# Kernel optimization log

Measured on AMD Instinct MI355X. Metric: run time of the kernel, lower is better.

The kernel has to match this reference:

```python
import jax, jax.numpy as jnp
import numpy as np

# --- SLAYER hyperparameters (from netParams) ---
THETA = 10.0        # spike threshold
TAU_SR = 10.0       # SRM alpha-kernel time constant (ms)
TAU_RHO = 1.0       # surrogate-gradient width
SCALE_RHO = 1.0     # surrogate-gradient scale
TS = 1.0            # simulation step (ms)
T_SAMPLE = 300      # number of time steps
K_LEN = 64          # truncated SRM kernel length

N_BATCH, N_IN, N_HID, N_OUT = 128, 784, 410, 10


def srm_kernel():
    # SRM-alpha kernel eps(t) = (t/tau) * exp(1 - t/tau), sampled at Ts, eps(0)=0
    t = jnp.arange(K_LEN, dtype=jnp.float32) * TS
    return (t / TAU_SR) * jnp.exp(1.0 - t / TAU_SR)


def psp(x):
    # Causal FIR filtering along time: out[t] = sum_k eps[k] * x[t-k]
    # x: [N, C, T]
    n, c, t = x.shape
    kern = srm_kernel()
    lhs = x.reshape(n * c, 1, t)
    rhs = kern[::-1].reshape(1, 1, K_LEN)  # flip: conv_general_dilated is cross-correlation
    out = jax.lax.conv_general_dilated(
        lhs, rhs, window_strides=(1,), padding=[(K_LEN - 1, 0)],
        dimension_numbers=("NCH", "OIH", "NCH"))
    return out.reshape(n, c, t)


@jax.custom_vjp
def spike_fn(u):
    # Heaviside threshold with surrogate gradient rho(u) = (scale/tau) * exp(-|u-theta|/tau)
    return (u >= THETA).astype(u.dtype)

def _spike_fwd(u):
    return spike_fn(u), u

def _spike_bwd(u, g):
    return (g * (SCALE_RHO / TAU_RHO) * jnp.exp(-jnp.abs(u - THETA) / TAU_RHO),)

spike_fn.defvjp(_spike_fwd, _spike_bwd)


def setup_inputs() -> dict:
    key = jax.random.key(0)
    k1, k2, k3, k4 = jax.random.split(key, 4)
    img = jax.random.uniform(k1, (N_BATCH, N_IN), dtype=jnp.float32)
    rand_u = jax.random.uniform(k2, (N_BATCH, N_IN, T_SAMPLE), dtype=jnp.float32)
    W1 = jax.random.normal(k3, (N_HID, N_IN), dtype=jnp.float32)
    W2 = jax.random.normal(k4, (N_OUT, N_HID), dtype=jnp.float32)
    return {"img": img, "rand_u": rand_u, "W1": W1, "W2": W2}


def reference(img, rand_u, W1, W2):
    # Poisson spike encoding: spike whenever uniform noise < pixel intensity
    s0 = (rand_u < img[:, :, None]).astype(jnp.float32)        # [N, 784, T]
    # fc1 (dense over spatial features, shared over time) -> psp -> spike
    a1 = jnp.einsum("nit,oi->not", s0, W1)                     # [N, 410, T]
    s1 = spike_fn(psp(a1))
    # fc2 -> psp -> spike
    a2 = jnp.einsum("nht,oh->not", s1, W2)                     # [N, 10, T]
    s2 = spike_fn(psp(a2))
    return s2
```

## Files before the change

### kernel.cpp

```cpp
#include <hip/hip_runtime.h>
#include <cstdint>
#include <cstddef>

#define N_B 128
#define N_I 784
#define N_H 410
#define N_O 10
#define TT  300
#define KL  64
#define NK  832
#define NKS 13
#define NTILES 26
#define NDIG 4
#define NKS2 7
#define S1_TILE 4800
#define S1_NSTRIDE 134400
#define SEGL 19
#define NWG1 (NTILES * N_B)
#define WPX  (NWG1 / 8)

typedef int v4i __attribute__((ext_vector_type(4)));

__global__ void k_pack(const float* __restrict__ rand_u, const float* __restrict__ img,
                       uint8_t* __restrict__ s0b) {
  int t = blockIdx.x * 64 + threadIdx.x;
  int w2 = blockIdx.y;
  int n = blockIdx.z;
  if (t >= TT) return;
  const float* rb = rand_u + (size_t)n * N_I * TT + t;
  const float* ib = img + (size_t)n * N_I;
  uint8_t* dst = s0b + ((size_t)n * TT + t) * NK + w2 * 64;
  int kb = w2 * 64;
  #pragma unroll
  for (int g = 0; g < 4; ++g) {
    uint32_t wd[4];
    #pragma unroll
    for (int q = 0; q < 4; ++q) {
      uint32_t v = 0;
      #pragma unroll
      for (int b = 0; b < 4; ++b) {
        int i = kb + g * 16 + q * 4 + b;
        float r = (i < N_I) ? rb[(size_t)i * TT] : 2.0f;
        float p = (i < N_I) ? ib[i] : 0.0f;
        v |= (r < p ? 1u : 0u) << (8 * b);
      }
      wd[q] = v;
    }
    v4i o; o[0] = (int)wd[0]; o[1] = (int)wd[1]; o[2] = (int)wd[2]; o[3] = (int)wd[3];
    *(v4i*)(dst + g * 16) = o;
  }
}

__global__ void k_bprepall(const float* __restrict__ W1, const float* __restrict__ W2,
                           v4i* __restrict__ Bf, v4i* __restrict__ Bf2) {
  int bid  = blockIdx.x;
  int lane = threadIdx.x;
  if (bid < NDIG * NTILES * NKS) {
    int ks   = bid % NKS;
    int rest = bid / NKS;
    int nt   = rest % NTILES;
    int d    = rest / NTILES;
    int o     = nt * 16 + (lane & 15);
    int kbase = ks * 64 + (lane >> 4) * 16;
    uint32_t wds[4] = {0, 0, 0, 0};
    for (int j = 0; j < 16; ++j) {
      int k = kbase + j;
      int dig = 0;
      if (o < N_H && k < N_I) {
        double w = (double)W1[(size_t)o * N_I + k];
        int r = (int)llround(w * 268435456.0);
        for (int dd = 0; dd <= d; ++dd) {
          dig = (int)(int8_t)(uint8_t)(r & 255);
          r = (r - dig) >> 8;
        }
      }
      wds[j >> 2] |= ((uint32_t)(uint8_t)(int8_t)dig) << (8 * (j & 3));
    }
    v4i v; v[0] = (int)wds[0]; v[1] = (int)wds[1]; v[2] = (int)wds[2]; v[3] = (int)wds[3];
    Bf[(size_t)bid * 64 + lane] = v;
  } else {
    int b2 = bid - NDIG * NTILES * NKS;
    int ks = b2 % NKS2, d = b2 / NKS2;
    int o     = lane & 15;
    int kbase = ks * 64 + (lane >> 4) * 16;
    uint32_t wds[4] = {0, 0, 0, 0};
    for (int j = 0; j < 16; ++j) {
      int k = kbase + j;
      int dig = 0;
      if (o < N_O && k < N_H) {
        double w = (double)W2[(size_t)o * N_H + k];
        int r = (int)llround(w * 268435456.0);
        for (int dd = 0; dd <= d; ++dd) {
          dig = (int)(int8_t)(uint8_t)(r & 255);
          r = (r - dig) >> 8;
        }
      }
      wds[j >> 2] |= ((uint32_t)(uint8_t)(int8_t)dig) << (8 * (j & 3));
    }
    v4i v; v[0] = (int)wds[0]; v[1] = (int)wds[1]; v[2] = (int)wds[2]; v[3] = (int)wds[3];
    Bf2[(size_t)b2 * 64 + lane] = v;
  }
}

__global__ __launch_bounds__(256) void k_fused2(const uint8_t* __restrict__ s0b,
                                                const v4i* __restrict__ Bf,
                                                uint8_t* __restrict__ s1) {
  __shared__ double tile[TT][17];
  int tid = threadIdx.x;
  int wave = tid >> 6, lane = tid & 63;
  int bid = blockIdx.x;
  int sw = (bid & 7) * WPX + (bid >> 3);
  int n = sw / NTILES, nt = sw % NTILES;
  int lrow = lane & 15, quad = lane >> 4;
  const v4i* bb = Bf + (size_t)nt * NKS * 64 + lane;
  const size_t dstr = (size_t)NTILES * NKS * 64;
  const uint8_t* an = s0b + (size_t)n * TT * NK + quad * 16;

  v4i acc[5][NDIG];
  #pragma unroll
  for (int mti = 0; mti < 5; ++mti)
    #pragma unroll
    for (int d = 0; d < NDIG; ++d) { acc[mti][d][0]=0; acc[mti][d][1]=0; acc[mti][d][2]=0; acc[mti][d][3]=0; }
  const uint8_t* ap[5];
  #pragma unroll
  for (int mti = 0; mti < 5; ++mti) {
    int rr = wave * 80 + mti * 16 + lrow;
    if (rr > TT - 1) rr = TT - 1;
    ap[mti] = an + (size_t)rr * NK;
  }
  v4i bcur[NDIG], acur[5];
  #pragma unroll
  for (int d = 0; d < NDIG; ++d) bcur[d] = bb[d * dstr];
  #pragma unroll
  for (int mti = 0; mti < 5; ++mti) acur[mti] = *(const v4i*)ap[mti];
  for (int ks = 0; ks < NKS; ++ks) {
    int ks2 = (ks + 1 < NKS) ? ks + 1 : ks;
    v4i bnxt[NDIG], anxt[5];
    #pragma unroll
    for (int d = 0; d < NDIG; ++d) bnxt[d] = bb[d * dstr + ks2 * 64];
    #pragma unroll
    for (int mti = 0; mti < 5; ++mti) anxt[mti] = *(const v4i*)(ap[mti] + ks2 * 64);
    #pragma unroll
    for (int mti = 0; mti < 5; ++mti)
      #pragma unroll
      for (int d = 0; d < NDIG; ++d)
        acc[mti][d] = __builtin_amdgcn_mfma_i32_16x16x64_i8(acur[mti], bcur[d], acc[mti][d], 0, 0, 0);
    #pragma unroll
    for (int d = 0; d < NDIG; ++d) bcur[d] = bnxt[d];
    #pragma unroll
    for (int mti = 0; mti < 5; ++mti) acur[mti] = anxt[mti];
  }
  #pragma unroll
  for (int mti = 0; mti < 5; ++mti)
    #pragma unroll
    for (int r = 0; r < 4; ++r) {
      int m = wave * 80 + mti * 16 + quad * 4 + r;
      if (m < TT) {
        double v = (double)acc[mti][0][r]
                 + 256.0      * (double)acc[mti][1][r]
                 + 65536.0    * (double)acc[mti][2][r]
                 + 16777216.0 * (double)acc[mti][3][r];
        tile[m][lrow] = v;
      }
    }
  __syncthreads();

  {
    int col = tid & 15;
    int seg = tid >> 4;
    int T0 = seg * SEGL;
    int Wc = T0 - 63; if (Wc < 0) Wc = 0;
    const double q   = exp(-0.1);
    const double q64 = exp(-6.4);
    const double cS  = (exp(1.0) / 10.0) * (1.0 / 268435456.0);
    double s1a = 0.0, s2a = 0.0, s1b = 0.0, s2b = 0.0;
    uint8_t* sb = s1 + (size_t)n * S1_NSTRIDE + (size_t)nt * S1_TILE + col;
    for (int j = 0; j < 63; ++j) {
      int t = T0 - 63 + j;
      int tc = (t < 0) ? 0 : t;
      double xa = (t >= 0) ? tile[tc][col] : 0.0;
      s2a = q * (s2a + s1a);
      s1a = q * s1a + xa;
    }
    for (int j = 0; j < SEGL; ++j) {
      int t = T0 + j;
      int tc = (t > TT - 1) ? TT - 1 : t;
      int tb = t - 64;
      int tbc = (tb < 0) ? 0 : tb;
      double xa = tile[tc][col];
      double xb = (tb >= Wc) ? tile[tbc][col] : 0.0;
      s2b = q * (s2b + s1b);
      s1b = q * s1b + xb;
      s2a = q * (s2a + s1a);
      s1a = q * s1a + xa;
      double y = cS * (s2a - q64 * (s2b + 64.0 * s1b));
      if (t < TT) sb[(size_t)t * 16] = (y >= 10.0) ? 1 : 0;
    }
  }
}

__global__ __launch_bounds__(256) void k_l2f(const uint8_t* __restrict__ s1,
                                             const v4i* __restrict__ Bf2,
                                             float* __restrict__ out) {
  __shared__ double tile2[TT][17];
  int tid = threadIdx.x;
  int wave = tid >> 6, lane = tid & 63;
  int n = blockIdx.x;
  int lrow = lane & 15, quad = lane >> 4;
  const uint8_t* s1n = s1 + (size_t)n * S1_NSTRIDE;
  for (int mt = wave; mt < 19; mt += 4) {
    int m0 = mt * 16;
    int trow = m0 + lrow; if (trow > TT - 1) trow = TT - 1;
    v4i acc[NDIG];
    #pragma unroll
    for (int d = 0; d < NDIG; ++d) { acc[d][0]=0; acc[d][1]=0; acc[d][2]=0; acc[d][3]=0; }
    for (int ks = 0; ks < NKS2; ++ks) {
      v4i af = *(const v4i*)(s1n + (size_t)(ks * 4 + quad) * S1_TILE + (size_t)trow * 16);
      #pragma unroll
      for (int d = 0; d < NDIG; ++d) {
        v4i bf = Bf2[(size_t)(d * NKS2 + ks) * 64 + lane];
        acc[d] = __builtin_amdgcn_mfma_i32_16x16x64_i8(af, bf, acc[d], 0, 0, 0);
      }
    }
    #pragma unroll
    for (int r = 0; r < 4; ++r) {
      int m = m0 + quad * 4 + r;
      if (m < TT && lrow < N_O) {
        double v = (double)acc[0][r]
                 + 256.0      * (double)acc[1][r]
                 + 65536.0    * (double)acc[2][r]
                 + 16777216.0 * (double)acc[3][r];
        tile2[m][lrow] = v;
      }
    }
  }
  __syncthreads();

  {
    int col = tid & 15;
    int seg = tid >> 4;
    int T0 = seg * SEGL;
    int Wc = T0 - 63; if (Wc < 0) Wc = 0;
    const double q   = exp(-0.1);
    const double q64 = exp(-6.4);
    const double cS  = (exp(1.0) / 10.0) * (1.0 / 268435456.0);
    double s1a = 0.0, s2a = 0.0, s1b = 0.0, s2b = 0.0;
    float* ob = out + (size_t)n * N_O * TT + (size_t)col * TT;
    for (int j = 0; j < 63; ++j) {
      int t = T0 - 63 + j;
      int tc = (t < 0) ? 0 : t;
      double xa = (t >= 0) ? tile2[tc][col] : 0.0;
      s2a = q * (s2a + s1a);
      s1a = q * s1a + xa;
    }
    for (int j = 0; j < SEGL; ++j) {
      int t = T0 + j;
      int tc = (t > TT - 1) ? TT - 1 : t;
      int tb = t - 64;
      int tbc = (tb < 0) ? 0 : tb;
      double xa = tile2[tc][col];
      double xb = (tb >= Wc) ? tile2[tbc][col] : 0.0;
      s2b = q * (s2b + s1b);
      s1b = q * s1b + xb;
      s2a = q * (s2a + s1a);
      s1a = q * s1a + xa;
      double y = cS * (s2a - q64 * (s2b + 64.0 * s1b));
      if (t < TT && col < N_O) ob[t] = (y >= 10.0) ? 1.0f : 0.0f;
    }
  }
}

extern "C" void kernel_launch(void* const* d_in, const int* in_sizes, int n_in,
                              void* d_out, int out_size, void* d_ws, size_t ws_size,
                              hipStream_t stream) {
  const float* img   = (const float*)d_in[0];
  const float* randu = (const float*)d_in[1];
  const float* W1    = (const float*)d_in[2];
  const float* W2    = (const float*)d_in[3];
  float* out = (float*)d_out;

  char* ws = (char*)d_ws;
  size_t off = 0;
  auto alloc = [&](size_t bytes) -> void* {
    void* p = ws + off;
    off = (off + bytes + 511) & ~(size_t)511;
    return p;
  };
  uint8_t*  s0b = (uint8_t*) alloc((size_t)N_B * TT * NK);
  v4i*      Bf  = (v4i*)     alloc((size_t)NDIG * NTILES * NKS * 64 * 16);
  v4i*      Bf2 = (v4i*)     alloc((size_t)NDIG * NKS2 * 64 * 16);
  uint8_t*  s1  = (uint8_t*) alloc((size_t)N_B * S1_NSTRIDE);
  if (off > ws_size) return;

  k_pack    <<<dim3(5, NKS, N_B), 64, 0, stream>>>(randu, img, s0b);
  k_bprepall<<<dim3(NDIG * NTILES * NKS + NDIG * NKS2), 64, 0, stream>>>(W1, W2, Bf, Bf2);
  k_fused2  <<<dim3(NWG1), 256, 0, stream>>>(s0b, Bf, s1);
  k_l2f     <<<dim3(N_B), 256, 0, stream>>>(s1, Bf2, out);
}
```

Measured before the change: 345.9 us.

## Stage layer-1 operands through LDS with async triple-buffered loads; split layer-2 blocks

The layer-1 int8 MFMA GEMM now fetches A and B fragments with global_load_lds (direct global-to-LDS copies) into double-parity LDS buffers, issued three K-steps ahead, and uses manual vmcnt/lgkmcnt waits so loads overlap the MFMA work. The shared tile buffer is reused as LDS staging, which increases LDS use to 72KB per block and may lower occupancy. Separately, the layer-2 kernel launches two blocks per batch item, each scanning half the time range, to double parallelism at the cost of recomputing the layer-2 GEMM in both halves. The hand-written waitcnt counts carry a correctness risk, since the buffer parity reuse depends on them being exact.

```diff
diff --git a/kernel.cpp b/kernel.cpp
--- a/kernel.cpp
+++ b/kernel.cpp
@@ -16,10 +16,18 @@
 #define S1_TILE 4800
 #define S1_NSTRIDE 134400
 #define SEGL 19
+#define SEGL2 10
 #define NWG1 (NTILES * N_B)
 #define WPX  (NWG1 / 8)
+#define DBYTES (NTILES * NKS * 1024)
 
 typedef int v4i __attribute__((ext_vector_type(4)));
+
+__device__ __forceinline__ void glds16(const void* g, void* l) {
+  __builtin_amdgcn_global_load_lds(
+      (const __attribute__((address_space(1))) uint32_t*)g,
+      (__attribute__((address_space(3))) uint32_t*)l, 16, 0, 0);
+}
 
 __global__ void k_pack(const float* __restrict__ rand_u, const float* __restrict__ img,
                        uint8_t* __restrict__ s0b) {
@@ -105,61 +113,97 @@
 __global__ __launch_bounds__(256) void k_fused2(const uint8_t* __restrict__ s0b,
                                                 const v4i* __restrict__ Bf,
                                                 uint8_t* __restrict__ s1) {
-  __shared__ double tile[TT][17];
+  __shared__ __align__(16) uint8_t smem[73728];
+  uint8_t* bufA = smem;
+  uint8_t* bufB = smem + 40960;
+  double (*tile)[17] = (double (*)[17])smem;
+
   int tid = threadIdx.x;
   int wave = tid >> 6, lane = tid & 63;
   int bid = blockIdx.x;
   int sw = (bid & 7) * WPX + (bid >> 3);
   int n = sw / NTILES, nt = sw % NTILES;
   int lrow = lane & 15, quad = lane >> 4;
-  const v4i* bb = Bf + (size_t)nt * NKS * 64 + lane;
-  const size_t dstr = (size_t)NTILES * NKS * 64;
-  const uint8_t* an = s0b + (size_t)n * TT * NK + quad * 16;
+
+  const uint8_t* an0 = s0b + (size_t)n * TT * NK;
+  int arow = wave * 80 + (lane >> 2);
+  int acol = (lane & 3) * 16;
+  const uint8_t* bfb = (const uint8_t*)Bf + (size_t)nt * NKS * 1024 + (size_t)lane * 16;
+
+  auto STAGE = [&](int k, int par) {
+    uint8_t* ad = bufA + par * 20480 + wave * 5120;
+    #pragma unroll
+    for (int c = 0; c < 5; ++c) {
+      int r = arow + c * 16; if (r > TT - 1) r = TT - 1;
+      glds16(an0 + (size_t)r * NK + (size_t)k * 64 + acol, ad + c * 1024);
+    }
+    uint8_t* bd = bufB + par * 16384 + wave * 4096;
+    #pragma unroll
+    for (int d = 0; d < NDIG; ++d)
+      glds16(bfb + (size_t)d * DBYTES + (size_t)k * 1024, bd + d * 1024);
+  };
+  auto LDA = [&](int par, v4i* a) {
+    const uint8_t* base = bufA + par * 20480 + wave * 5120 + quad * 16;
+    #pragma unroll
+    for (int m = 0; m < 5; ++m)
+      a[m] = *(const v4i*)(base + (size_t)(m * 16 + lrow) * 64);
+  };
+  auto LDB = [&](int par, v4i* b) {
+    const uint8_t* base = bufB + par * 16384 + wave * 4096 + lane * 16;
+    #pragma unroll
+    for (int d = 0; d < NDIG; ++d)
+      b[d] = *(const v4i*)(base + (size_t)d * 1024);
+  };
 
   v4i acc[5][NDIG];
   #pragma unroll
-  for (int mti = 0; mti < 5; ++mti)
-    #pragma unroll
-    for (int d = 0; d < NDIG; ++d) { acc[mti][d][0]=0; acc[mti][d][1]=0; acc[mti][d][2]=0; acc[mti][d][3]=0; }
-  const uint8_t* ap[5];
+  for (int m = 0; m < 5; ++m)
+    #pragma unroll
+    for (int d = 0; d < NDIG; ++d) { acc[m][d][0]=0; acc[m][d][1]=0; acc[m][d][2]=0; acc[m][d][3]=0; }
+
+  STAGE(0, 0);
+  STAGE(1, 1);
+  asm volatile("s_waitcnt vmcnt(9)" ::: "memory");
+  v4i acur[5], bcur[NDIG], anxt[5], bnxt[NDIG];
+  LDA(0, acur); LDB(0, bcur);
+  asm volatile("s_waitcnt lgkmcnt(0)" ::: "memory");
+  __builtin_amdgcn_sched_barrier(0);
+  STAGE(2, 0);
+
   #pragma unroll
-  for (int mti = 0; mti < 5; ++mti) {
-    int rr = wave * 80 + mti * 16 + lrow;
-    if (rr > TT - 1) rr = TT - 1;
-    ap[mti] = an + (size_t)rr * NK;
-  }
-  v4i bcur[NDIG], acur[5];
+  for (int ks = 0; ks < NKS; ++ks) {
+    if (ks < NKS - 2) { asm volatile("s_waitcnt vmcnt(9)" ::: "memory"); }
+    else              { asm volatile("s_waitcnt vmcnt(0)" ::: "memory"); }
+    int pn = (ks + 1) & 1;
+    if (ks < NKS - 1) { LDA(pn, anxt); LDB(pn, bnxt); }
+    #pragma unroll
+    for (int m = 0; m < 5; ++m)
+      #pragma unroll
+      for (int d = 0; d < NDIG; ++d)
+        acc[m][d] = __builtin_amdgcn_mfma_i32_16x16x64_i8(acur[m], bcur[d], acc[m][d], 0, 0, 0);
+    asm volatile("s_waitcnt lgkmcnt(0)" ::: "memory");
+    __builtin_amdgcn_sched_barrier(0);
+    if (ks < NKS - 3) STAGE(ks + 3, (ks + 3) & 1);
+    if (ks < NKS - 1) {
+      #pragma unroll
+      for (int m = 0; m < 5; ++m) acur[m] = anxt[m];
+      #pragma unroll
+      for (int d = 0; d < NDIG; ++d) bcur[d] = bnxt[d];
+    }
+  }
+
+  __syncthreads();
+
   #pragma unroll
-  for (int d = 0; d < NDIG; ++d) bcur[d] = bb[d * dstr];
-  #pragma unroll
-  for (int mti = 0; mti < 5; ++mti) acur[mti] = *(const v4i*)ap[mti];
-  for (int ks = 0; ks < NKS; ++ks) {
-    int ks2 = (ks + 1 < NKS) ? ks + 1 : ks;
-    v4i bnxt[NDIG], anxt[5];
-    #pragma unroll
-    for (int d = 0; d < NDIG; ++d) bnxt[d] = bb[d * dstr + ks2 * 64];
-    #pragma unroll
-    for (int mti = 0; mti < 5; ++mti) anxt[mti] = *(const v4i*)(ap[mti] + ks2 * 64);
-    #pragma unroll
-    for (int mti = 0; mti < 5; ++mti)
-      #pragma unroll
-      for (int d = 0; d < NDIG; ++d)
-        acc[mti][d] = __builtin_amdgcn_mfma_i32_16x16x64_i8(acur[mti], bcur[d], acc[mti][d], 0, 0, 0);
-    #pragma unroll
-    for (int d = 0; d < NDIG; ++d) bcur[d] = bnxt[d];
-    #pragma unroll
-    for (int mti = 0; mti < 5; ++mti) acur[mti] = anxt[mti];
-  }
-  #pragma unroll
-  for (int mti = 0; mti < 5; ++mti)
+  for (int m5 = 0; m5 < 5; ++m5)
     #pragma unroll
     for (int r = 0; r < 4; ++r) {
-      int m = wave * 80 + mti * 16 + quad * 4 + r;
+      int m = wave * 80 + m5 * 16 + quad * 4 + r;
       if (m < TT) {
-        double v = (double)acc[mti][0][r]
-                 + 256.0      * (double)acc[mti][1][r]
-                 + 65536.0    * (double)acc[mti][2][r]
-                 + 16777216.0 * (double)acc[mti][3][r];
+        double v = (double)acc[m5][0][r]
+                 + 256.0      * (double)acc[m5][1][r]
+                 + 65536.0    * (double)acc[m5][2][r]
+                 + 16777216.0 * (double)acc[m5][3][r];
         tile[m][lrow] = v;
       }
     }
@@ -205,7 +249,7 @@
   __shared__ double tile2[TT][17];
   int tid = threadIdx.x;
   int wave = tid >> 6, lane = tid & 63;
-  int n = blockIdx.x;
+  int half = blockIdx.x, n = blockIdx.y;
   int lrow = lane & 15, quad = lane >> 4;
   const uint8_t* s1n = s1 + (size_t)n * S1_NSTRIDE;
   for (int mt = wave; mt < 19; mt += 4) {
@@ -238,8 +282,8 @@
 
   {
     int col = tid & 15;
-    int seg = tid >> 4;
-    int T0 = seg * SEGL;
+    int seg = half * 16 + (tid >> 4);
+    int T0 = seg * SEGL2;
     int Wc = T0 - 63; if (Wc < 0) Wc = 0;
     const double q   = exp(-0.1);
     const double q64 = exp(-6.4);
@@ -249,15 +293,17 @@
     for (int j = 0; j < 63; ++j) {
       int t = T0 - 63 + j;
       int tc = (t < 0) ? 0 : t;
-      double xa = (t >= 0) ? tile2[tc][col] : 0.0;
+      tc = (tc > TT - 1) ? TT - 1 : tc;
+      double xa = (t >= 0 && t < TT) ? tile2[tc][col] : 0.0;
       s2a = q * (s2a + s1a);
       s1a = q * s1a + xa;
     }
-    for (int j = 0; j < SEGL; ++j) {
+    for (int j = 0; j < SEGL2; ++j) {
       int t = T0 + j;
       int tc = (t > TT - 1) ? TT - 1 : t;
       int tb = t - 64;
       int tbc = (tb < 0) ? 0 : tb;
+      tbc = (tbc > TT - 1) ? TT - 1 : tbc;
       double xa = tile2[tc][col];
       double xb = (tb >= Wc) ? tile2[tbc][col] : 0.0;
       s2b = q * (s2b + s1b);
@@ -295,5 +341,5 @@
   k_pack    <<<dim3(5, NKS, N_B), 64, 0, stream>>>(randu, img, s0b);
   k_bprepall<<<dim3(NDIG * NTILES * NKS + NDIG * NKS2), 64, 0, stream>>>(W1, W2, Bf, Bf2);
   k_fused2  <<<dim3(NWG1), 256, 0, stream>>>(s0b, Bf, s1);
-  k_l2f     <<<dim3(N_B), 256, 0, stream>>>(s1, Bf2, out);
-}
+  k_l2f     <<<dim3(2, N_B), 256, 0, stream>>>(s1, Bf2, out);
+}
```

After: 311.6 us. -9.9%, faster.
